# Kernel optimization log

Measured on AMD Instinct MI355X. Metric: run time of the kernel, lower is better.

## Reference

```python
import jax, jax.numpy as jnp
import numpy as np

N_NODES = 100000


def gcn_conv(x, src, dst, W, b, n_nodes):
    # PyG GCNConv: h = x @ W; add self-loops; symmetric norm; scatter-add; + bias
    h = x @ W  # [N, F_out]
    deg = jax.ops.segment_sum(jnp.ones_like(src, dtype=h.dtype), dst, num_segments=n_nodes)
    dinv = jnp.where(deg > 0, jax.lax.rsqrt(deg), 0.0)
    norm = dinv[src] * dinv[dst]  # [E+N]
    msgs = h[src] * norm[:, None]  # gather + scale
    out = jax.ops.segment_sum(msgs, dst, num_segments=n_nodes)  # scatter-add
    return out + b


def setup_inputs() -> dict:
    key = jax.random.key(0)
    ks = jax.random.split(key, 8)
    n, e, f_in, h = N_NODES, 1600000, 128, 64
    x = jax.random.normal(ks[0], (n, f_in), dtype=jnp.float32)
    edge_index = jax.random.randint(ks[1], (2, e), 0, n, dtype=jnp.int64)
    W1 = jax.random.normal(ks[2], (f_in, h), dtype=jnp.float32) / np.sqrt(f_in)
    b1 = jnp.zeros((h,), dtype=jnp.float32)
    W2 = jax.random.normal(ks[3], (h, h), dtype=jnp.float32) / np.sqrt(h)
    b2 = jnp.zeros((h,), dtype=jnp.float32)
    Wd = jax.random.normal(ks[4], (h, 1), dtype=jnp.float32) / np.sqrt(h)
    bd = jnp.zeros((1,), dtype=jnp.float32)
    return {"x": x, "edge_index": edge_index, "W1": W1, "b1": b1,
            "W2": W2, "b2": b2, "Wd": Wd, "bd": bd}


def reference(x, edge_index, W1, b1, W2, b2, Wd, bd):
    n = x.shape[0]
    loop = jnp.arange(n, dtype=edge_index.dtype)
    src = jnp.concatenate([edge_index[0], loop])  # add self-loops once
    dst = jnp.concatenate([edge_index[1], loop])
    h = jax.nn.relu(gcn_conv(x, src, dst, W1, b1, n))
    h = jax.nn.relu(gcn_conv(h, src, dst, W2, b2, n))
    return h @ Wd + bd
```

## Files before the change

kernel.cpp:

```cpp
#include <hip/hip_runtime.h>

#define NF 64
#define NBLK 256
#define SH 8
#define BMSK 255
#define MAXNB 2048

typedef unsigned short ushort_t;
typedef __attribute__((ext_vector_type(8))) short short8;
typedef __attribute__((ext_vector_type(4))) float f32x4;

__device__ inline ushort_t f2bf(float f) {
    unsigned u = __float_as_uint(f);
    return (ushort_t)((u + 0x7fffu + ((u >> 16) & 1u)) >> 16);
}
__device__ inline float bfhi(unsigned x) { return __uint_as_float(x & 0xffff0000u); }
__device__ inline float bflo(unsigned x) { return __uint_as_float(x << 16); }

#define PACK8(b, ua, ub) \
    b[0] = (short)f2bf(ua.x); b[1] = (short)f2bf(ua.y); \
    b[2] = (short)f2bf(ua.z); b[3] = (short)f2bf(ua.w); \
    b[4] = (short)f2bf(ub.x); b[5] = (short)f2bf(ub.y); \
    b[6] = (short)f2bf(ub.z); b[7] = (short)f2bf(ub.w);


__device__ inline int wave_incl_scan(int x, int lane) {
#pragma unroll
    for (int o = 1; o < 64; o <<= 1) { int y = __shfl_up(x, o, 64); if (lane >= o) x += y; }
    return x;
}

__global__ __launch_bounds__(256) void k_scan_a(const int* __restrict__ in, int* __restrict__ out,
                                                int* __restrict__ bsums, int n) {
    int t = threadIdx.x, lane = t & 63, wv = t >> 6;
    int base = blockIdx.x * 1024 + t * 4;
    int v[4]; int s = 0;
#pragma unroll
    for (int k = 0; k < 4; ++k) { int i = base + k; int x = (i < n) ? in[i] : 0; v[k] = s; s += x; }
    int incl = wave_incl_scan(s, lane);
    __shared__ int ws[4];
    if (lane == 63) ws[wv] = incl;
    __syncthreads();
    int wofs = 0;
#pragma unroll
    for (int w = 0; w < 4; ++w) if (w < wv) wofs += ws[w];
    int texcl = wofs + incl - s;
#pragma unroll
    for (int k = 0; k < 4; ++k) { int i = base + k; if (i < n) out[i] = texcl + v[k]; }
    if (t == 255) bsums[blockIdx.x] = wofs + incl;
}

__global__ __launch_bounds__(256) void k_scan_small(const int* __restrict__ cnt, int* __restrict__ ptr, int NB) {
    int t = threadIdx.x, lane = t & 63, wv = t >> 6;
    int base = t * 8;
    int local[8]; int s = 0;
#pragma unroll
    for (int k = 0; k < 8; ++k) { int i = base + k; int x = (i < NB) ? cnt[i] : 0; local[k] = s; s += x; }
    int incl = wave_incl_scan(s, lane);
    __shared__ int ws[4];
    if (lane == 63) ws[wv] = incl;
    __syncthreads();
    int wofs = 0;
#pragma unroll
    for (int w = 0; w < 4; ++w) if (w < wv) wofs += ws[w];
    int texcl = wofs + incl - s;
#pragma unroll
    for (int k = 0; k < 8; ++k) { int i = base + k; if (i < NB) ptr[i] = texcl + local[k]; }
}

__global__ __launch_bounds__(256) void k_scan_addb(int* __restrict__ data, const int* __restrict__ bsums,
                                                   int* __restrict__ bptr, int ntot, int E) {
    int i = blockIdx.x * 256 + threadIdx.x;
    if (i < ntot) {
        int v = data[i] + bsums[i >> 10];
        data[i] = v;
        if ((i & (NBLK - 1)) == 0) bptr[i / NBLK] = v;
    }
    if (i == 0) bptr[ntot / NBLK] = E;
}


__global__ __launch_bounds__(256) void k_histA(const int* __restrict__ dst, int* __restrict__ hmat,
                                               int E, int NB, int chunk) {
    __shared__ int h[MAXNB];
    int blk = blockIdx.x;
    for (int i = threadIdx.x; i < NB; i += 256) h[i] = 0;
    __syncthreads();
    int beg = blk * chunk, end = beg + chunk; if (end > E) end = E;
    for (int e = beg + threadIdx.x; e < end; e += 256) atomicAdd(&h[dst[e] >> SH], 1);
    __syncthreads();
    for (int i = threadIdx.x; i < NB; i += 256) hmat[i * NBLK + blk] = h[i];
}

__global__ __launch_bounds__(256) void k_placeB(const int* __restrict__ src, const int* __restrict__ dst,
                                                const int* __restrict__ hmat, int* __restrict__ pairs,
                                                int E, int NB, int chunk) {
    __shared__ int cur[MAXNB];
    int blk = blockIdx.x;
    for (int i = threadIdx.x; i < NB; i += 256) cur[i] = hmat[i * NBLK + blk];
    __syncthreads();
    int beg = blk * chunk, end = beg + chunk; if (end > E) end = E;
    for (int e = beg + threadIdx.x; e < end; e += 256) {
        int s = src[e], d = dst[e];
        int off = atomicAdd(&cur[d >> SH], 1);
        pairs[off] = (s << SH) | (d & BMSK);
    }
}

__global__ __launch_bounds__(256) void k_csr(const int* __restrict__ bptr, const int* __restrict__ pairs,
                                             int* __restrict__ row_ptr, int* __restrict__ cnt,
                                             float* __restrict__ dinv, int* __restrict__ col, int n) {
    __shared__ int h[256];
    __shared__ int cur[256];
    __shared__ int ws[4];
    int b = blockIdx.x, t = threadIdx.x;
    h[t] = 0;
    __syncthreads();
    int beg = bptr[b], end = bptr[b + 1];
    for (int j = beg + t; j < end; j += 256) atomicAdd(&h[pairs[j] & BMSK], 1);
    __syncthreads();
    int c = h[t];
    int incl = wave_incl_scan(c, t & 63);
    if ((t & 63) == 63) ws[t >> 6] = incl;
    __syncthreads();
    int wofs = 0;
#pragma unroll
    for (int w = 0; w < 4; ++w) if (w < (t >> 6)) wofs += ws[w];
    int ex = wofs + incl - c;
    int node = (b << SH) + t;
    if (node < n) {
        row_ptr[node] = beg + ex;
        cnt[node] = c;
        dinv[node] = rsqrtf(1.0f + (float)c);
    }
    cur[t] = beg + ex;
    __syncthreads();
    for (int j = beg + t; j < end; j += 256) {
        int pk = pairs[j];
        int p = atomicAdd(&cur[pk & BMSK], 1);
        col[p] = pk >> SH;
    }
}

__global__ __launch_bounds__(256) void k_mm1(
    const float* __restrict__ X, const float* __restrict__ W,
    const float* __restrict__ dinv, ushort_t* __restrict__ out, int n)
{
    __shared__ ushort_t wf[16 * 512];
    int t = threadIdx.x;
    for (int idx = t; idx < 128 * 64; idx += 256) {
        int k = idx >> 6, c = idx & 63;
        int f = ((k >> 5) << 2) | (c >> 4);
        int ln = (c & 15) | (((k >> 3) & 3) << 4);
        wf[f * 512 + ln * 8 + (k & 7)] = f2bf(W[idx]);
    }
    __syncthreads();

    int lane = t & 63, wv = t >> 6;
    int r16 = lane & 15, kg = lane >> 4;
    int tile = blockIdx.x * 4 + wv;
    int row = tile * 16 + r16;
    int r = (row < n) ? row : (n - 1);
    const float* pX = X + (size_t)r * 128 + kg * 8;

    float4 u0a = *(const float4*)(pX + 0),   u0b = *(const float4*)(pX + 4);
    float4 u1a = *(const float4*)(pX + 32),  u1b = *(const float4*)(pX + 36);
    float4 u2a = *(const float4*)(pX + 64),  u2b = *(const float4*)(pX + 68);
    float4 u3a = *(const float4*)(pX + 96),  u3b = *(const float4*)(pX + 100);

    short8 b0, b1, b2, b3;
    PACK8(b0, u0a, u0b); PACK8(b1, u1a, u1b);
    PACK8(b2, u2a, u2b); PACK8(b3, u3a, u3b);

    short8 a0[4], a1[4], a2[4], a3[4];
#pragma unroll
    for (int f = 0; f < 4; ++f) {
        a0[f] = *(const short8*)(wf + (0 + f) * 512 + lane * 8);
        a1[f] = *(const short8*)(wf + (4 + f) * 512 + lane * 8);
        a2[f] = *(const short8*)(wf + (8 + f) * 512 + lane * 8);
        a3[f] = *(const short8*)(wf + (12 + f) * 512 + lane * 8);
    }

    f32x4 z = {0.f, 0.f, 0.f, 0.f};
    f32x4 acc[4];
#pragma unroll
    for (int f = 0; f < 4; ++f)
        acc[f] = __builtin_amdgcn_mfma_f32_16x16x32_bf16(a0[f], b0, z, 0, 0, 0);
#pragma unroll
    for (int f = 0; f < 4; ++f)
        acc[f] = __builtin_amdgcn_mfma_f32_16x16x32_bf16(a1[f], b1, acc[f], 0, 0, 0);
#pragma unroll
    for (int f = 0; f < 4; ++f)
        acc[f] = __builtin_amdgcn_mfma_f32_16x16x32_bf16(a2[f], b2, acc[f], 0, 0, 0);
#pragma unroll
    for (int f = 0; f < 4; ++f)
        acc[f] = __builtin_amdgcn_mfma_f32_16x16x32_bf16(a3[f], b3, acc[f], 0, 0, 0);

    if (row < n) {
        float di = dinv[row];
#pragma unroll
        for (int f = 0; f < 4; ++f) {
            ushort4 o;
            o.x = f2bf(acc[f][0] * di); o.y = f2bf(acc[f][1] * di);
            o.z = f2bf(acc[f][2] * di); o.w = f2bf(acc[f][3] * di);
            *(ushort4*)(out + (size_t)row * NF + f * 16 + kg * 4) = o;
        }
    }
}

__global__ __launch_bounds__(256) void k_mm2(
    const ushort_t* __restrict__ Xb, const float* __restrict__ W,
    const float* __restrict__ dinv, ushort_t* __restrict__ out, int n)
{
    __shared__ ushort_t wf[8 * 512];
    int t = threadIdx.x;
    for (int idx = t; idx < 64 * 64; idx += 256) {
        int k = idx >> 6, c = idx & 63;
        int f = ((k >> 5) << 2) | (c >> 4);
        int ln = (c & 15) | (((k >> 3) & 3) << 4);
        wf[f * 512 + ln * 8 + (k & 7)] = f2bf(W[idx]);
    }
    __syncthreads();

    int lane = t & 63, wv = t >> 6;
    short8 af[8];
#pragma unroll
    for (int f = 0; f < 8; ++f)
        af[f] = *(const short8*)(wf + f * 512 + lane * 8);

    int r16 = lane & 15, kg = lane >> 4;
    int tile0 = blockIdx.x * 8 + wv * 2;
    int rowA = tile0 * 16 + r16;
    int rowB = rowA + 16;
    int rA = (rowA < n) ? rowA : (n - 1);
    int rB = (rowB < n) ? rowB : (n - 1);

    const ushort_t* pA = Xb + (size_t)rA * NF + kg * 8;
    const ushort_t* pB = Xb + (size_t)rB * NF + kg * 8;
    short8 bA0 = *(const short8*)(pA);
    short8 bA1 = *(const short8*)(pA + 32);
    short8 bB0 = *(const short8*)(pB);
    short8 bB1 = *(const short8*)(pB + 32);

    f32x4 z = {0.f, 0.f, 0.f, 0.f};
    f32x4 accA[4], accB[4];
#pragma unroll
    for (int f = 0; f < 4; ++f) {
        accA[f] = __builtin_amdgcn_mfma_f32_16x16x32_bf16(af[f], bA0, z, 0, 0, 0);
        accA[f] = __builtin_amdgcn_mfma_f32_16x16x32_bf16(af[4 + f], bA1, accA[f], 0, 0, 0);
        accB[f] = __builtin_amdgcn_mfma_f32_16x16x32_bf16(af[f], bB0, z, 0, 0, 0);
        accB[f] = __builtin_amdgcn_mfma_f32_16x16x32_bf16(af[4 + f], bB1, accB[f], 0, 0, 0);
    }

    if (rowA < n) {
        float di = dinv[rowA];
#pragma unroll
        for (int f = 0; f < 4; ++f) {
            ushort4 o;
            o.x = f2bf(accA[f][0] * di); o.y = f2bf(accA[f][1] * di);
            o.z = f2bf(accA[f][2] * di); o.w = f2bf(accA[f][3] * di);
            *(ushort4*)(out + (size_t)rowA * NF + f * 16 + kg * 4) = o;
        }
    }
    if (rowB < n) {
        float di = dinv[rowB];
#pragma unroll
        for (int f = 0; f < 4; ++f) {
            ushort4 o;
            o.x = f2bf(accB[f][0] * di); o.y = f2bf(accB[f][1] * di);
            o.z = f2bf(accB[f][2] * di); o.w = f2bf(accB[f][3] * di);
            *(ushort4*)(out + (size_t)rowB * NF + f * 16 + kg * 4) = o;
        }
    }
}

template<bool DECODE>
__global__ __launch_bounds__(256) void k_pull(
    const ushort_t* __restrict__ hs, const float* __restrict__ dinv,
    const int* __restrict__ row_ptr, const int* __restrict__ cnt,
    const int* __restrict__ col, const float* __restrict__ bias,
    const float* __restrict__ Wd, const float* __restrict__ bd,
    void* __restrict__ outv, int n)
{
    int d = blockIdx.x * 16 + (threadIdx.x >> 4);
    if (d >= n) return;
    int lt = threadIdx.x & 15;
    int fo = lt << 2;
    int grpbase = threadIdx.x & 48;
    int beg = row_ptr[d], deg = cnt[d];

    uint2 sv = *((const uint2*)(hs + (size_t)d * NF) + lt);
    float4 acc = make_float4(bflo(sv.x), bfhi(sv.x), bflo(sv.y), bfhi(sv.y));

    for (int jb = 0; jb < deg; jb += 16) {
        int m = deg - jb; if (m > 16) m = 16;
        int idx = (lt < m) ? col[beg + jb + lt] : 0;
        uint2 v[16];
#pragma unroll
        for (int u = 0; u < 16; ++u) {
            int kk = (u < m) ? u : (m - 1);
            int s = __shfl(idx, grpbase + kk, 64);
            v[u] = *((const uint2*)(hs + (size_t)s * NF) + lt);
        }
#pragma unroll
        for (int u = 0; u < 16; ++u) {
            if (u < m) {
                acc.x += bflo(v[u].x); acc.y += bfhi(v[u].x);
                acc.z += bflo(v[u].y); acc.w += bfhi(v[u].y);
            }
        }
    }

    float di = dinv[d];
    float4 bv = *(const float4*)(bias + fo);
    float rx = fmaxf(fmaf(acc.x, di, bv.x), 0.0f);
    float ry = fmaxf(fmaf(acc.y, di, bv.y), 0.0f);
    float rz = fmaxf(fmaf(acc.z, di, bv.z), 0.0f);
    float rw = fmaxf(fmaf(acc.w, di, bv.w), 0.0f);

    if (DECODE) {
        float4 wv = *(const float4*)(Wd + fo);
        float vsum = rx * wv.x + ry * wv.y + rz * wv.z + rw * wv.w;
#pragma unroll
        for (int o = 1; o < 16; o <<= 1) vsum += __shfl_xor(vsum, o, 64);
        if (lt == 0) ((float*)outv)[d] = vsum + bd[0];
    } else {
        ushort4 o;
        o.x = f2bf(rx); o.y = f2bf(ry); o.z = f2bf(rz); o.w = f2bf(rw);
        *(ushort4*)((ushort_t*)outv + (size_t)d * NF + fo) = o;
    }
}

extern "C" void kernel_launch(void* const* d_in, const int* in_sizes, int n_in,
                              void* d_out, int out_size, void* d_ws, size_t ws_size,
                              hipStream_t stream) {
    const float* x  = (const float*)d_in[0];
    const int*   ei = (const int*)d_in[1];
    const float* W1 = (const float*)d_in[2];
    const float* b1 = (const float*)d_in[3];
    const float* W2 = (const float*)d_in[4];
    const float* b2 = (const float*)d_in[5];
    const float* Wd = (const float*)d_in[6];
    const float* bd = (const float*)d_in[7];
    float* out = (float*)d_out;

    int n = in_sizes[0] / 128;
    int E = in_sizes[1] / 2;
    const int* src = ei;
    const int* dst = ei + E;

    int NB = (n + (1 << SH) - 1) >> SH;
    int chunk = (E + NBLK - 1) / NBLK;
    int ntot = NB * NBLK;
    int nsb = (ntot + 1023) / 1024;
    int ntiles = (n + 15) / 16;

    float* dinv    = (float*)d_ws;
    float* bufH    = dinv + n;
    float* bufA    = bufH + (size_t)n * NF;
    int*   counts  = (int*)(bufA + (size_t)n * NF);
    int*   row_ptr = counts + n;
    int*   col     = row_ptr + n;
    int*   hmat    = col + E;
    int*   bptr    = hmat + ntot;
    int*   bsums   = bptr + NB + 1;
    int*   pairs   = (int*)bufH;
    ushort_t* hsb  = (ushort_t*)bufH;
    ushort_t* actb = (ushort_t*)bufA;

    k_histA<<<NBLK, 256, 0, stream>>>(dst, hmat, E, NB, chunk);
    k_scan_a<<<nsb, 256, 0, stream>>>(hmat, hmat, bsums, ntot);
    k_scan_small<<<1, 256, 0, stream>>>(bsums, bsums, nsb);
    k_scan_addb<<<(ntot + 255) / 256, 256, 0, stream>>>(hmat, bsums, bptr, ntot, E);
    k_placeB<<<NBLK, 256, 0, stream>>>(src, dst, hmat, pairs, E, NB, chunk);

    k_csr<<<NB, 256, 0, stream>>>(bptr, pairs, row_ptr, counts, dinv, col, n);

    k_mm1<<<(ntiles + 3) / 4, 256, 0, stream>>>(x, W1, dinv, hsb, n);
    k_pull<false><<<(n + 15) / 16, 256, 0, stream>>>(hsb, dinv, row_ptr, counts, col, b1,
                                                     Wd, bd, actb, n);

    k_mm2<<<(ntiles + 7) / 8, 256, 0, stream>>>(actb, W2, dinv, hsb, n);
    k_pull<true><<<(n + 15) / 16, 256, 0, stream>>>(hsb, dinv, row_ptr, counts, col, b2,
                                                    Wd, bd, out, n);
}
```

Measured before the change: 142.8 us.

## Fuse CSR build pipeline into one cooperative kernel with grid syncs

Replaces the six CSR-construction kernels (histogram, three-pass scan, placement, per-bucket CSR) with a single cooperative kernel that uses grid-wide syncs between phases, and restructures the scan as a per-bucket row scan plus a small scan of bucket totals. The aim is to remove several launch gaps and the separate multi-level scan kernels. In exchange, the CSR phase is limited to 256 blocks, which loop over buckets, so it has less parallelism than the previous one-block-per-bucket launch. Grid syncs also add their own barrier cost.

```diff
diff --git a/kernel.cpp b/kernel.cpp
--- a/kernel.cpp
+++ b/kernel.cpp
@@ -1,4 +1,7 @@
 #include <hip/hip_runtime.h>
+#include <hip/hip_cooperative_groups.h>
+
+namespace cg = cooperative_groups;
 
 #define NF 64
 #define NBLK 256
@@ -23,122 +26,104 @@
     b[4] = (short)f2bf(ub.x); b[5] = (short)f2bf(ub.y); \
     b[6] = (short)f2bf(ub.z); b[7] = (short)f2bf(ub.w);
 
-
 __device__ inline int wave_incl_scan(int x, int lane) {
 #pragma unroll
     for (int o = 1; o < 64; o <<= 1) { int y = __shfl_up(x, o, 64); if (lane >= o) x += y; }
     return x;
 }
 
-__global__ __launch_bounds__(256) void k_scan_a(const int* __restrict__ in, int* __restrict__ out,
-                                                int* __restrict__ bsums, int n) {
-    int t = threadIdx.x, lane = t & 63, wv = t >> 6;
-    int base = blockIdx.x * 1024 + t * 4;
-    int v[4]; int s = 0;
-#pragma unroll
-    for (int k = 0; k < 4; ++k) { int i = base + k; int x = (i < n) ? in[i] : 0; v[k] = s; s += x; }
-    int incl = wave_incl_scan(s, lane);
+__global__ __launch_bounds__(256) void k_build(
+    const int* __restrict__ src, const int* __restrict__ dst,
+    int* __restrict__ hmat, int* __restrict__ tsum, int* __restrict__ bptr,
+    int* __restrict__ pairs, int* __restrict__ row_ptr, int* __restrict__ cnt,
+    float* __restrict__ dinv, int* __restrict__ col,
+    int n, int E, int NB, int chunk)
+{
+    cg::grid_group grid = cg::this_grid();
+    int blk = blockIdx.x, t = threadIdx.x;
+    int G = gridDim.x;
+    int lane = t & 63, wv = t >> 6;
+    __shared__ int h[MAXNB];
     __shared__ int ws[4];
-    if (lane == 63) ws[wv] = incl;
-    __syncthreads();
-    int wofs = 0;
-#pragma unroll
-    for (int w = 0; w < 4; ++w) if (w < wv) wofs += ws[w];
-    int texcl = wofs + incl - s;
-#pragma unroll
-    for (int k = 0; k < 4; ++k) { int i = base + k; if (i < n) out[i] = texcl + v[k]; }
-    if (t == 255) bsums[blockIdx.x] = wofs + incl;
-}
-
-__global__ __launch_bounds__(256) void k_scan_small(const int* __restrict__ cnt, int* __restrict__ ptr, int NB) {
-    int t = threadIdx.x, lane = t & 63, wv = t >> 6;
-    int base = t * 8;
-    int local[8]; int s = 0;
-#pragma unroll
-    for (int k = 0; k < 8; ++k) { int i = base + k; int x = (i < NB) ? cnt[i] : 0; local[k] = s; s += x; }
-    int incl = wave_incl_scan(s, lane);
-    __shared__ int ws[4];
-    if (lane == 63) ws[wv] = incl;
-    __syncthreads();
-    int wofs = 0;
-#pragma unroll
-    for (int w = 0; w < 4; ++w) if (w < wv) wofs += ws[w];
-    int texcl = wofs + incl - s;
-#pragma unroll
-    for (int k = 0; k < 8; ++k) { int i = base + k; if (i < NB) ptr[i] = texcl + local[k]; }
-}
-
-__global__ __launch_bounds__(256) void k_scan_addb(int* __restrict__ data, const int* __restrict__ bsums,
-                                                   int* __restrict__ bptr, int ntot, int E) {
-    int i = blockIdx.x * 256 + threadIdx.x;
-    if (i < ntot) {
-        int v = data[i] + bsums[i >> 10];
-        data[i] = v;
-        if ((i & (NBLK - 1)) == 0) bptr[i / NBLK] = v;
-    }
-    if (i == 0) bptr[ntot / NBLK] = E;
-}
-
-
-__global__ __launch_bounds__(256) void k_histA(const int* __restrict__ dst, int* __restrict__ hmat,
-                                               int E, int NB, int chunk) {
-    __shared__ int h[MAXNB];
-    int blk = blockIdx.x;
-    for (int i = threadIdx.x; i < NB; i += 256) h[i] = 0;
-    __syncthreads();
+
     int beg = blk * chunk, end = beg + chunk; if (end > E) end = E;
-    for (int e = beg + threadIdx.x; e < end; e += 256) atomicAdd(&h[dst[e] >> SH], 1);
-    __syncthreads();
-    for (int i = threadIdx.x; i < NB; i += 256) hmat[i * NBLK + blk] = h[i];
-}
-
-__global__ __launch_bounds__(256) void k_placeB(const int* __restrict__ src, const int* __restrict__ dst,
-                                                const int* __restrict__ hmat, int* __restrict__ pairs,
-                                                int E, int NB, int chunk) {
-    __shared__ int cur[MAXNB];
-    int blk = blockIdx.x;
-    for (int i = threadIdx.x; i < NB; i += 256) cur[i] = hmat[i * NBLK + blk];
-    __syncthreads();
-    int beg = blk * chunk, end = beg + chunk; if (end > E) end = E;
-    for (int e = beg + threadIdx.x; e < end; e += 256) {
+
+    for (int i = t; i < NB; i += 256) h[i] = 0;
+    __syncthreads();
+    for (int e = beg + t; e < end; e += 256) atomicAdd(&h[dst[e] >> SH], 1);
+    __syncthreads();
+    for (int i = t; i < NB; i += 256) hmat[i * NBLK + blk] = h[i];
+    grid.sync();
+
+    for (int b = blk; b < NB; b += G) {
+        int c = hmat[b * NBLK + t];
+        int incl = wave_incl_scan(c, lane);
+        if (lane == 63) ws[wv] = incl;
+        __syncthreads();
+        int wofs = 0;
+#pragma unroll
+        for (int w = 0; w < 4; ++w) if (w < wv) wofs += ws[w];
+        hmat[b * NBLK + t] = wofs + incl - c;
+        if (t == 255) tsum[b] = wofs + incl;
+        __syncthreads();
+    }
+    grid.sync();
+
+    if (blk == 0) {
+        int base = t * 8;
+        int local[8]; int s = 0;
+#pragma unroll
+        for (int k = 0; k < 8; ++k) { int i = base + k; int x = (i < NB) ? tsum[i] : 0; local[k] = s; s += x; }
+        int incl = wave_incl_scan(s, lane);
+        if (lane == 63) ws[wv] = incl;
+        __syncthreads();
+        int wofs = 0;
+#pragma unroll
+        for (int w = 0; w < 4; ++w) if (w < wv) wofs += ws[w];
+        int texcl = wofs + incl - s;
+#pragma unroll
+        for (int k = 0; k < 8; ++k) { int i = base + k; if (i < NB) bptr[i] = texcl + local[k]; }
+        if (t == 0) bptr[NB] = E;
+    }
+    grid.sync();
+
+    for (int i = t; i < NB; i += 256) h[i] = hmat[i * NBLK + blk] + bptr[i];
+    __syncthreads();
+    for (int e = beg + t; e < end; e += 256) {
         int s = src[e], d = dst[e];
-        int off = atomicAdd(&cur[d >> SH], 1);
+        int off = atomicAdd(&h[d >> SH], 1);
         pairs[off] = (s << SH) | (d & BMSK);
     }
-}
-
-__global__ __launch_bounds__(256) void k_csr(const int* __restrict__ bptr, const int* __restrict__ pairs,
-                                             int* __restrict__ row_ptr, int* __restrict__ cnt,
-                                             float* __restrict__ dinv, int* __restrict__ col, int n) {
-    __shared__ int h[256];
-    __shared__ int cur[256];
-    __shared__ int ws[4];
-    int b = blockIdx.x, t = threadIdx.x;
-    h[t] = 0;
-    __syncthreads();
-    int beg = bptr[b], end = bptr[b + 1];
-    for (int j = beg + t; j < end; j += 256) atomicAdd(&h[pairs[j] & BMSK], 1);
-    __syncthreads();
-    int c = h[t];
-    int incl = wave_incl_scan(c, t & 63);
-    if ((t & 63) == 63) ws[t >> 6] = incl;
-    __syncthreads();
-    int wofs = 0;
-#pragma unroll
-    for (int w = 0; w < 4; ++w) if (w < (t >> 6)) wofs += ws[w];
-    int ex = wofs + incl - c;
-    int node = (b << SH) + t;
-    if (node < n) {
-        row_ptr[node] = beg + ex;
-        cnt[node] = c;
-        dinv[node] = rsqrtf(1.0f + (float)c);
-    }
-    cur[t] = beg + ex;
-    __syncthreads();
-    for (int j = beg + t; j < end; j += 256) {
-        int pk = pairs[j];
-        int p = atomicAdd(&cur[pk & BMSK], 1);
-        col[p] = pk >> SH;
+    grid.sync();
+
+    for (int b = blk; b < NB; b += G) {
+        int bbeg = bptr[b], bend = bptr[b + 1];
+        h[t] = 0;
+        __syncthreads();
+        for (int j = bbeg + t; j < bend; j += 256) atomicAdd(&h[pairs[j] & BMSK], 1);
+        __syncthreads();
+        int c = h[t];
+        int incl = wave_incl_scan(c, lane);
+        if (lane == 63) ws[wv] = incl;
+        __syncthreads();
+        int wofs = 0;
+#pragma unroll
+        for (int w = 0; w < 4; ++w) if (w < wv) wofs += ws[w];
+        int ex = wofs + incl - c;
+        int node = (b << SH) + t;
+        if (node < n) {
+            row_ptr[node] = bbeg + ex;
+            cnt[node] = c;
+            dinv[node] = rsqrtf(1.0f + (float)c);
+        }
+        h[256 + t] = bbeg + ex;
+        __syncthreads();
+        for (int j = bbeg + t; j < bend; j += 256) {
+            int pk = pairs[j];
+            int p = atomicAdd(&h[256 + (pk & BMSK)], 1);
+            col[p] = pk >> SH;
+        }
+        __syncthreads();
     }
 }
 
@@ -352,7 +337,6 @@
     int NB = (n + (1 << SH) - 1) >> SH;
     int chunk = (E + NBLK - 1) / NBLK;
     int ntot = NB * NBLK;
-    int nsb = (ntot + 1023) / 1024;
     int ntiles = (n + 15) / 16;
 
     float* dinv    = (float*)d_ws;
@@ -363,18 +347,15 @@
     int*   col     = row_ptr + n;
     int*   hmat    = col + E;
     int*   bptr    = hmat + ntot;
-    int*   bsums   = bptr + NB + 1;
+    int*   tsum    = bptr + NB + 1;
     int*   pairs   = (int*)bufH;
     ushort_t* hsb  = (ushort_t*)bufH;
     ushort_t* actb = (ushort_t*)bufA;
 
-    k_histA<<<NBLK, 256, 0, stream>>>(dst, hmat, E, NB, chunk);
-    k_scan_a<<<nsb, 256, 0, stream>>>(hmat, hmat, bsums, ntot);
-    k_scan_small<<<1, 256, 0, stream>>>(bsums, bsums, nsb);
-    k_scan_addb<<<(ntot + 255) / 256, 256, 0, stream>>>(hmat, bsums, bptr, ntot, E);
-    k_placeB<<<NBLK, 256, 0, stream>>>(src, dst, hmat, pairs, E, NB, chunk);
-
-    k_csr<<<NB, 256, 0, stream>>>(bptr, pairs, row_ptr, counts, dinv, col, n);
+    void* args[] = {(void*)&src, (void*)&dst, (void*)&hmat, (void*)&tsum, (void*)&bptr,
+                    (void*)&pairs, (void*)&row_ptr, (void*)&counts, (void*)&dinv,
+                    (void*)&col, (void*)&n, (void*)&E, (void*)&NB, (void*)&chunk};
+    hipLaunchCooperativeKernel((const void*)k_build, dim3(NBLK), dim3(256), args, 0, stream);
 
     k_mm1<<<(ntiles + 3) / 4, 256, 0, stream>>>(x, W1, dinv, hsb, n);
     k_pull<false><<<(n + 15) / 16, 256, 0, stream>>>(hsb, dinv, row_ptr, counts, col, b1,
```

Result: slower. 282.5 us (+97.8%).
